# Performance work log

Hardware: AMD Instinct MI355X
Metric: run time of the kernel (lower is better)

Reference implementation:

```python
import jax, jax.numpy as jnp
import numpy as np

N = 50000; E = 800000; H = 4; C = 64; FEAT = 128; EDIM = 16; G = 256
NEG_SLOPE = 0.2; BN_EPS = 1e-5


def _gat_layer(x, src, dst, W, a_src, a_dst, bias, gamma, beta, alpha_edge=None):
    # GATConv (concat=True, PyG math), then BatchNorm1d (batch stats) + ReLU.
    h = (x @ W).reshape(N, H, C)                       # [N,H,C]
    alpha = (h * a_src).sum(-1)[src] + (h * a_dst).sum(-1)[dst]   # [Etot,H]
    if alpha_edge is not None:
        alpha = alpha + alpha_edge
    alpha = jax.nn.leaky_relu(alpha, NEG_SLOPE)
    amax = jax.ops.segment_max(alpha, dst, num_segments=N)        # edge softmax over dst
    ea = jnp.exp(alpha - amax[dst])
    denom = jax.ops.segment_sum(ea, dst, num_segments=N)
    coef = ea / (denom[dst] + 1e-16)
    out = jax.ops.segment_sum(coef[:, :, None] * h[src], dst, num_segments=N)
    out = out.reshape(N, H * C) + bias
    mu = out.mean(0)
    var = out.var(0)
    out = (out - mu) / jnp.sqrt(var + BN_EPS) * gamma + beta
    return jax.nn.relu(out)


def setup_inputs() -> dict:
    key = jax.random.key(0)
    ks = jax.random.split(key, 32)
    s = 0.05
    inp = {
        "x": jax.random.normal(ks[0], (N, FEAT), jnp.float32),
        "edge_index": jax.random.randint(ks[1], (2, E), 0, N),
        "edge_attr": jax.random.normal(ks[2], (E, EDIM), jnp.float32),
        "batch": jnp.sort(jax.random.randint(ks[3], (N,), 0, G)),
    }
    in_dims = [FEAT, H * C, H * C]
    for i in range(3):
        k = 4 + 7 * i
        inp[f"W{i}"] = jax.random.normal(ks[k], (in_dims[i], H * C), jnp.float32) * s
        inp[f"att_src{i}"] = jax.random.normal(ks[k + 1], (H, C), jnp.float32) * s
        inp[f"att_dst{i}"] = jax.random.normal(ks[k + 2], (H, C), jnp.float32) * s
        inp[f"bias{i}"] = jnp.zeros((H * C,), jnp.float32)
        inp[f"gamma{i}"] = jnp.ones((H * C,), jnp.float32)
        inp[f"beta{i}"] = jnp.zeros((H * C,), jnp.float32)
    inp["We0"] = jax.random.normal(ks[28], (EDIM, H * C), jnp.float32) * s
    inp["att_e0"] = jax.random.normal(ks[29], (H, C), jnp.float32) * s
    return inp


def reference(x, edge_index, edge_attr, batch,
              W0, att_src0, att_dst0, bias0, gamma0, beta0,
              W1, att_src1, att_dst1, bias1, gamma1, beta1,
              W2, att_src2, att_dst2, bias2, gamma2, beta2,
              We0, att_e0):
    # PyG GATConv adds self-loops; edge_attr for self-loops filled with mean.
    loops = jnp.arange(N)
    src = jnp.concatenate([edge_index[0], loops])
    dst = jnp.concatenate([edge_index[1], loops])
    ea_sl = jnp.concatenate([edge_attr, jnp.broadcast_to(edge_attr.mean(0), (N, EDIM))], 0)
    e = (ea_sl @ We0).reshape(E + N, H, C)
    alpha_e = (e * att_e0).sum(-1)                     # [Etot,H]
    x = _gat_layer(x, src, dst, W0, att_src0, att_dst0, bias0, gamma0, beta0, alpha_e)
    x = _gat_layer(x, src, dst, W1, att_src1, att_dst1, bias1, gamma1, beta1)
    x = _gat_layer(x, src, dst, W2, att_src2, att_dst2, bias2, gamma2, beta2)
    # global_mean_pool
    counts = jax.ops.segment_sum(jnp.ones((N,), x.dtype), batch, num_segments=G)
    sums = jax.ops.segment_sum(x, batch, num_segments=G)
    return sums / jnp.clip(counts, 1.0)[:, None]
```

## Files before the change

### kernel.cpp

```cpp
#include <hip/hip_runtime.h>
#include <math.h>

#define NN 50000
#define NE 800000
#define ET 850000
#define HCC 256
#define GG 256
#define CAP 64
#define NB 16

constexpr int RTILES = 782;
constexpr int G0B    = 512;
constexpr int CSRB   = 416;

constexpr size_t NHC    = (size_t)NN * HCC;
constexpr size_t O_H    = 0;
constexpr size_t O_AGG  = O_H + NHC / 2;
constexpr size_t O_REC  = O_AGG + NHC / 2;
constexpr size_t O_BT0  = O_REC + (size_t)NN * CAP * 4;
constexpr size_t O_BT1  = O_BT0 + 16384;
constexpr size_t O_BT2  = O_BT1 + 32768;
constexpr size_t O_AS   = O_BT2 + 32768;
constexpr size_t O_AD   = O_AS + (size_t)NN * 4;
constexpr size_t O_M    = O_AD + (size_t)NN * 4;
constexpr size_t O_ZERO = O_M + 64;
constexpr size_t O_DEG  = O_ZERO;
constexpr size_t O_SLS  = O_DEG + NN;
constexpr size_t O_PART = O_SLS + 4;
constexpr size_t O_END  = O_PART + 3 * NB * 512;
constexpr size_t ZWORDS = O_END - O_ZERO;
constexpr int    ZBLK   = (int)((ZWORDS / 4 + 255) / 256);

typedef __attribute__((ext_vector_type(8))) short bf16x8;
typedef __attribute__((ext_vector_type(4))) float f32x4;

__device__ inline unsigned short f2bf(float f) {
    unsigned int u = __float_as_uint(f);
    unsigned int r = (u + 0x7fffu + ((u >> 16) & 1u)) >> 16;
    return (unsigned short)r;
}
__device__ inline float b2f(unsigned short u) {
    return __uint_as_float(((unsigned int)u) << 16);
}
__device__ inline float bflo(unsigned int u) { return __uint_as_float(u << 16); }
__device__ inline float bfhi(unsigned int u) { return __uint_as_float(u & 0xffff0000u); }

__global__ void prep_kernel(const float* __restrict__ W0, const float* __restrict__ W1,
                            const float* __restrict__ W2,
                            const float* __restrict__ We0, const float* __restrict__ att_e0,
                            unsigned short* __restrict__ Bt0,
                            unsigned short* __restrict__ Bt1,
                            unsigned short* __restrict__ Bt2,
                            float* __restrict__ M, float* __restrict__ zbase) {
    int b = blockIdx.x;
    if (b >= 641) {
        size_t idx = ((size_t)(b - 641) * 256 + threadIdx.x) * 4;
        if (idx < ZWORDS)
            *(float4*)(zbase + idx) = make_float4(0.f, 0.f, 0.f, 0.f);
        return;
    }
    if (b == 640) {
        int t = threadIdx.x;
        if (t < 64) {
            int k = t >> 2, hh = t & 3;
            float s = 0.f;
            for (int c = 0; c < 64; ++c)
                s += We0[k * 256 + hh * 64 + c] * att_e0[hh * 64 + c];
            M[k * 4 + hh] = s;
        }
        return;
    }
    const float* W; unsigned short* Bt; int K, base;
    if (b < 128)      { W = W0; Bt = Bt0; K = 128; base = 0; }
    else if (b < 384) { W = W1; Bt = Bt1; K = 256; base = 128; }
    else              { W = W2; Bt = Bt2; K = 256; base = 384; }
    int idx = (b - base) * 256 + threadIdx.x;
    int n = idx & 255, k = idx >> 8;
    Bt[(size_t)n * K + k] = f2bf(W[(size_t)k * 256 + n]);
}

__global__ __launch_bounds__(512) void g0csr(const float* __restrict__ xf,
                                             const unsigned short* __restrict__ Bt,
                                             const float* __restrict__ att_src,
                                             const float* __restrict__ att_dst,
                                             unsigned short* __restrict__ Hout,
                                             float* __restrict__ asA,
                                             float* __restrict__ adA,
                                             const int* __restrict__ srcA,
                                             const int* __restrict__ dstA,
                                             const float* __restrict__ ea,
                                             const float* __restrict__ Mm,
                                             int* __restrict__ deg,
                                             uint4* __restrict__ rec,
                                             float* __restrict__ slsum) {
    constexpr int K  = 128;
    constexpr int KP = K + 8;
    __shared__ unsigned short Bs[128][KP];
    __shared__ unsigned short As[2][64][KP];
    __shared__ float prt[8][4];

    int tid = threadIdx.x;
    int wave = tid >> 6, lane = tid & 63;

    if (blockIdx.x >= G0B) {
        int t0 = (int)(blockIdx.x - G0B) * 2048 + tid;
        float a0 = 0.f, a1 = 0.f, a2 = 0.f, a3 = 0.f;
        #pragma unroll
        for (int q = 0; q < 4; ++q) {
            int e = t0 + q * 512;
            if (e < ET) {
                bool real = (e < NE);
                int d = real ? dstA[e] : (e - NE);
                int s = real ? srcA[e] : (e - NE);
                int p = atomicAdd(&deg[d], 1);
                if (p > CAP - 1) p = CAP - 1;
                int slot = d * CAP + p;
                uint4 r;
                r.z = (unsigned)s;
                if (real) {
                    r.w = 0u;
                    const float4* pp = (const float4*)(ea + (size_t)e * 16);
                    float4 va = pp[0], vb = pp[1], vc = pp[2], vd = pp[3];
                    float v[16] = {va.x, va.y, va.z, va.w, vb.x, vb.y, vb.z, vb.w,
                                   vc.x, vc.y, vc.z, vc.w, vd.x, vd.y, vd.z, vd.w};
                    float o0 = 0.f, o1 = 0.f, o2 = 0.f, o3 = 0.f;
                    #pragma unroll
                    for (int k = 0; k < 16; ++k) {
                        float4 m4 = *(const float4*)(Mm + k * 4);
                        o0 = fmaf(v[k], m4.x, o0);
                        o1 = fmaf(v[k], m4.y, o1);
                        o2 = fmaf(v[k], m4.z, o2);
                        o3 = fmaf(v[k], m4.w, o3);
                    }
                    r.x = ((unsigned)f2bf(o1) << 16) | (unsigned)f2bf(o0);
                    r.y = ((unsigned)f2bf(o3) << 16) | (unsigned)f2bf(o2);
                    a0 += o0; a1 += o1; a2 += o2; a3 += o3;
                } else {
                    r.x = 0u; r.y = 0u; r.w = 1u;
                }
                rec[slot] = r;
            }
        }
        #pragma unroll
        for (int off = 32; off; off >>= 1) {
            a0 += __shfl_xor(a0, off);
            a1 += __shfl_xor(a1, off);
            a2 += __shfl_xor(a2, off);
            a3 += __shfl_xor(a3, off);
        }
        if (lane == 0) {
            prt[wave][0] = a0; prt[wave][1] = a1;
            prt[wave][2] = a2; prt[wave][3] = a3;
        }
        __syncthreads();
        if (tid < 4) {
            float s = 0.f;
            #pragma unroll
            for (int w = 0; w < 8; ++w) s += prt[w][tid];
            atomicAdd(&slsum[tid], s);
        }
        return;
    }

    int quad = lane >> 4, l16 = lane & 15;
    int wr = wave >> 1, wc = wave & 1;

    int b = blockIdx.x;
    int cb = (b >> 3) & 1;
    int ts = ((b >> 4) << 3) | (b & 7);
    const int np = G0B >> 1;
    int colbase = cb * 128;
    int head = cb * 2 + wc;

    {
        constexpr int TOT = 128 * K;
        for (int idx = tid * 8; idx < TOT; idx += 4096) {
            int br = idx / K, bk = idx % K;
            uint4 v = *(const uint4*)(Bt + (size_t)(colbase + br) * K + bk);
            *(uint4*)&Bs[br][bk] = v;
        }
    }

    int srow = tid >> 3;
    const int scol0 = (tid & 7) * 16;

    float4 ldA_[4], ldB_[4];

    auto issue = [&](float4 (&ld)[4], int t) {
        int r = t * 64 + srow;
        if (r < NN) {
            const float4* src = (const float4*)(xf + (size_t)r * K + scol0);
            #pragma unroll
            for (int q = 0; q < 4; ++q) ld[q] = src[q];
        } else {
            #pragma unroll
            for (int q = 0; q < 4; ++q) ld[q] = make_float4(0.f, 0.f, 0.f, 0.f);
        }
    };
    auto commit = [&](float4 (&ld)[4], int buf) {
        #pragma unroll
        for (int q = 0; q < 2; ++q) {
            float4 a = ld[2 * q], c = ld[2 * q + 1];
            uint4 v;
            v.x = ((unsigned)f2bf(a.y) << 16) | f2bf(a.x);
            v.y = ((unsigned)f2bf(a.w) << 16) | f2bf(a.z);
            v.z = ((unsigned)f2bf(c.y) << 16) | f2bf(c.x);
            v.w = ((unsigned)f2bf(c.w) << 16) | f2bf(c.z);
            *(uint4*)&As[buf][srow][scol0 + q * 8] = v;
        }
    };

    float asc[4], adc_[4];
    #pragma unroll
    for (int ni = 0; ni < 4; ++ni) {
        int c = colbase + wc * 64 + ni * 16 + l16;
        asc[ni]  = att_src[c];
        adc_[ni] = att_dst[c];
    }

    int t = ts;
    issue(ldA_, t);
    asm volatile("s_waitcnt lgkmcnt(0)" ::: "memory");
    __builtin_amdgcn_s_barrier();

    auto tilestep = [&](float4 (&ldCur)[4], float4 (&ldNxt)[4], int buf, int t_, int tn) {
        if (tn < RTILES) issue(ldNxt, tn);
        commit(ldCur, buf);
        asm volatile("s_waitcnt lgkmcnt(0)" ::: "memory");
        __builtin_amdgcn_s_barrier();

        f32x4 acc[4] = {};
        #pragma unroll
        for (int k0 = 0; k0 < K; k0 += 32) {
            bf16x8 af, bfr[4];
            af = *(const bf16x8*)&As[buf][wr * 16 + l16][k0 + quad * 8];
            #pragma unroll
            for (int ni = 0; ni < 4; ++ni)
                bfr[ni] = *(const bf16x8*)&Bs[wc * 64 + ni * 16 + l16][k0 + quad * 8];
            #pragma unroll
            for (int ni = 0; ni < 4; ++ni)
                acc[ni] = __builtin_amdgcn_mfma_f32_16x16x32_bf16(
                    af, bfr[ni], acc[ni], 0, 0, 0);
        }
        int row0 = t_ * 64 + wr * 16;
        #pragma unroll
        for (int reg = 0; reg < 4; ++reg) {
            int r = row0 + quad * 4 + reg;
            if (r < NN) {
                #pragma unroll
                for (int ni = 0; ni < 4; ++ni) {
                    int c = colbase + wc * 64 + ni * 16 + l16;
                    Hout[(size_t)r * HCC + c] = f2bf(acc[ni][reg]);
                }
            }
            float s1 = acc[0][reg] * asc[0] + acc[1][reg] * asc[1] +
                       acc[2][reg] * asc[2] + acc[3][reg] * asc[3];
            float d1 = acc[0][reg] * adc_[0] + acc[1][reg] * adc_[1] +
                       acc[2][reg] * adc_[2] + acc[3][reg] * adc_[3];
            #pragma unroll
            for (int off = 1; off < 16; off <<= 1) {
                s1 += __shfl_xor(s1, off);
                d1 += __shfl_xor(d1, off);
            }
            if (l16 == 0 && r < NN) {
                asA[(size_t)r * 4 + head] = s1;
                adA[(size_t)r * 4 + head] = d1;
            }
        }
    };

    while (t < RTILES) {
        int t1 = t + np;
        tilestep(ldA_, ldB_, 0, t, t1);
        t = t1;
        if (t >= RTILES) break;
        int t2 = t + np;
        tilestep(ldB_, ldA_, 1, t, t2);
        t = t2;
    }
}

template <int K, bool NORM>
__global__ __launch_bounds__(512) void gemm2(const unsigned short* __restrict__ Ab,
                                             const unsigned short* __restrict__ Bt,
                                             const float* __restrict__ part,
                                             const float* __restrict__ gamma,
                                             const float* __restrict__ beta,
                                             const float* __restrict__ att_src,
                                             const float* __restrict__ att_dst,
                                             unsigned short* __restrict__ Hout,
                                             float* __restrict__ asA,
                                             float* __restrict__ adA, int M) {
    constexpr int KP  = K + 8;
    constexpr int NLD = K / 64;
    __shared__ unsigned short Bs[128][KP];
    __shared__ unsigned short As[2][64][KP];
    __shared__ float kvs[256], cvs[256];

    int tid = threadIdx.x;
    int wave = tid >> 6, lane = tid & 63;
    int quad = lane >> 4, l16 = lane & 15;
    int wr = wave >> 1, wc = wave & 1;

    int b = blockIdx.x;
    int cb = (b >> 3) & 1;
    int ts = ((b >> 4) << 3) | (b & 7);
    int np = (int)(gridDim.x >> 1);
    int colbase = cb * 128;
    int head = cb * 2 + wc;

    if (NORM) {
        if (tid < 256) {
            int ch = tid;
            float s = 0.f, s2 = 0.f;
            #pragma unroll
            for (int q = 0; q < NB; ++q) {
                s  += part[q * 512 + ch];
                s2 += part[q * 512 + 256 + ch];
            }
            const float invN = 1.0f / (float)NN;
            float mr = s * invN;
            float var = s2 * invN - mr * mr;
            float k = gamma[ch] * rsqrtf(var + 1e-5f);
            kvs[ch] = k;
            cvs[ch] = beta[ch] - mr * k;
        }
    }
    {
        constexpr int TOT = 128 * K;
        for (int idx = tid * 8; idx < TOT; idx += 4096) {
            int br = idx / K, bk = idx % K;
            uint4 v = *(const uint4*)(Bt + (size_t)(colbase + br) * K + bk);
            *(uint4*)&Bs[br][bk] = v;
        }
    }

    int srow = tid >> 3;
    const int scol0 = (tid & 7) * (K / 8);

    uint4 ldA_[NLD], ldB_[NLD];

    auto issue = [&](uint4 (&ld)[NLD], int t) {
        int r = t * 64 + srow;
        if (r < M) {
            const uint4* src = (const uint4*)(Ab + (size_t)r * K + scol0);
            #pragma unroll
            for (int q = 0; q < NLD; ++q) ld[q] = src[q];
        } else {
            #pragma unroll
            for (int q = 0; q < NLD; ++q) ld[q] = make_uint4(0u, 0u, 0u, 0u);
        }
    };
    auto commit = [&](uint4 (&ld)[NLD], int buf) {
        #pragma unroll
        for (int q = 0; q < NLD; ++q) {
            uint4 v = ld[q];
            if (NORM) {
                int ch = scol0 + q * 8;
                float u[8] = {bflo(v.x), bfhi(v.x), bflo(v.y), bfhi(v.y),
                              bflo(v.z), bfhi(v.z), bflo(v.w), bfhi(v.w)};
                #pragma unroll
                for (int j = 0; j < 8; ++j)
                    u[j] = fmaxf(fmaf(u[j], kvs[ch + j], cvs[ch + j]), 0.f);
                v.x = ((unsigned)f2bf(u[1]) << 16) | f2bf(u[0]);
                v.y = ((unsigned)f2bf(u[3]) << 16) | f2bf(u[2]);
                v.z = ((unsigned)f2bf(u[5]) << 16) | f2bf(u[4]);
                v.w = ((unsigned)f2bf(u[7]) << 16) | f2bf(u[6]);
            }
            *(uint4*)&As[buf][srow][scol0 + q * 8] = v;
        }
    };

    float asc[4], adc_[4];
    #pragma unroll
    for (int ni = 0; ni < 4; ++ni) {
        int c = colbase + wc * 64 + ni * 16 + l16;
        asc[ni]  = att_src[c];
        adc_[ni] = att_dst[c];
    }

    int t = ts;
    issue(ldA_, t);
    asm volatile("s_waitcnt lgkmcnt(0)" ::: "memory");
    __builtin_amdgcn_s_barrier();

    auto tilestep = [&](uint4 (&ldCur)[NLD], uint4 (&ldNxt)[NLD], int buf, int t_, int tn) {
        if (tn < RTILES) issue(ldNxt, tn);
        commit(ldCur, buf);
        asm volatile("s_waitcnt lgkmcnt(0)" ::: "memory");
        __builtin_amdgcn_s_barrier();

        f32x4 acc[4] = {};
        #pragma unroll
        for (int k0 = 0; k0 < K; k0 += 32) {
            bf16x8 af, bfr[4];
            af = *(const bf16x8*)&As[buf][wr * 16 + l16][k0 + quad * 8];
            #pragma unroll
            for (int ni = 0; ni < 4; ++ni)
                bfr[ni] = *(const bf16x8*)&Bs[wc * 64 + ni * 16 + l16][k0 + quad * 8];
            #pragma unroll
            for (int ni = 0; ni < 4; ++ni)
                acc[ni] = __builtin_amdgcn_mfma_f32_16x16x32_bf16(
                    af, bfr[ni], acc[ni], 0, 0, 0);
        }
        int row0 = t_ * 64 + wr * 16;
        #pragma unroll
        for (int reg = 0; reg < 4; ++reg) {
            int r = row0 + quad * 4 + reg;
            if (r < M) {
                #pragma unroll
                for (int ni = 0; ni < 4; ++ni) {
                    int c = colbase + wc * 64 + ni * 16 + l16;
                    Hout[(size_t)r * HCC + c] = f2bf(acc[ni][reg]);
                }
            }
            float s1 = acc[0][reg] * asc[0] + acc[1][reg] * asc[1] +
                       acc[2][reg] * asc[2] + acc[3][reg] * asc[3];
            float d1 = acc[0][reg] * adc_[0] + acc[1][reg] * adc_[1] +
                       acc[2][reg] * adc_[2] + acc[3][reg] * adc_[3];
            #pragma unroll
            for (int off = 1; off < 16; off <<= 1) {
                s1 += __shfl_xor(s1, off);
                d1 += __shfl_xor(d1, off);
            }
            if (l16 == 0 && r < M) {
                asA[(size_t)r * 4 + head] = s1;
                adA[(size_t)r * 4 + head] = d1;
            }
        }
    };

    while (t < RTILES) {
        int t1 = t + np;
        tilestep(ldA_, ldB_, 0, t, t1);
        t = t1;
        if (t >= RTILES) break;
        int t2 = t + np;
        tilestep(ldB_, ldA_, 1, t, t2);
        t = t2;
    }
}

template <bool HAS_AE>
__global__ __launch_bounds__(512) void agg_kernel(const unsigned short* __restrict__ Hm,
                                                  const float* __restrict__ asA,
                                                  const float* __restrict__ adA,
                                                  const uint4* __restrict__ rec,
                                                  const int* __restrict__ degA,
                                                  const float* __restrict__ slsum,
                                                  unsigned short* __restrict__ outA,
                                                  float* __restrict__ part) {
    __shared__ float wlds[8][260];
    __shared__ float slds[2][8][256];
    int wave = threadIdx.x >> 6, lane = threadIdx.x & 63;
    int n = blockIdx.x * 8 + wave;
    int head = lane >> 4;
    int st = n * CAP;
    int d = degA[n];
    if (d > CAP) d = CAP;
    float4 ad4 = *(const float4*)(adA + (size_t)n * 4);

    float4 w4 = make_float4(0.f, 0.f, 0.f, 0.f);
    int ms = 0;
    if (lane < d) {
        uint4 r = rec[st + lane];
        ms = (int)r.z;
        float4 av = *(const float4*)(asA + (size_t)ms * 4);
        float4 t = make_float4(av.x + ad4.x, av.y + ad4.y, av.z + ad4.z, av.w + ad4.w);
        if (HAS_AE) {
            if (r.w) {
                const float inv = 1.0f / (float)NE;
                t.x += slsum[0] * inv; t.y += slsum[1] * inv;
                t.z += slsum[2] * inv; t.w += slsum[3] * inv;
            } else {
                t.x += bflo(r.x); t.y += bfhi(r.x);
                t.z += bflo(r.y); t.w += bfhi(r.y);
            }
        }
        t.x = (t.x > 0.f) ? t.x : 0.2f * t.x;
        t.y = (t.y > 0.f) ? t.y : 0.2f * t.y;
        t.z = (t.z > 0.f) ? t.z : 0.2f * t.z;
        t.w = (t.w > 0.f) ? t.w : 0.2f * t.w;
        w4.x = __expf(t.x);
        w4.y = __expf(t.y);
        w4.z = __expf(t.z);
        w4.w = __expf(t.w);
    }
    float4 Dv = w4;
    wlds[wave][0 * 65 + lane] = w4.x;
    wlds[wave][1 * 65 + lane] = w4.y;
    wlds[wave][2 * 65 + lane] = w4.z;
    wlds[wave][3 * 65 + lane] = w4.w;

    float4 acc = make_float4(0.f, 0.f, 0.f, 0.f);
    const unsigned short* hb = Hm + lane * 4;
    int cnt8 = (d + 7) & ~7;
    const float* wrow = &wlds[wave][head * 65];

    int sjA[8]; ushort4 hvA[8];
    #pragma unroll
    for (int q = 0; q < 8; ++q)
        sjA[q] = __builtin_amdgcn_readlane(ms, q);
    #pragma unroll
    for (int q = 0; q < 8; ++q)
        hvA[q] = *(const ushort4*)(hb + (size_t)sjA[q] * HCC);
    for (int jj = 0; jj < cnt8; jj += 8) {
        int nj = jj + 8;
        bool more = (nj < cnt8);
        ushort4 hvB[8];
        if (more) {
            int sjB[8];
            #pragma unroll
            for (int q = 0; q < 8; ++q)
                sjB[q] = __builtin_amdgcn_readlane(ms, nj + q);
            #pragma unroll
            for (int q = 0; q < 8; ++q)
                hvB[q] = *(const ushort4*)(hb + (size_t)sjB[q] * HCC);
        }
        float wq[8];
        #pragma unroll
        for (int q = 0; q < 8; ++q)
            wq[q] = wrow[jj + q];
        #pragma unroll
        for (int q = 0; q < 8; ++q) {
            acc.x = fmaf(wq[q], b2f(hvA[q].x), acc.x);
            acc.y = fmaf(wq[q], b2f(hvA[q].y), acc.y);
            acc.z = fmaf(wq[q], b2f(hvA[q].z), acc.z);
            acc.w = fmaf(wq[q], b2f(hvA[q].w), acc.w);
        }
        if (more) {
            #pragma unroll
            for (int q = 0; q < 8; ++q)
                hvA[q] = hvB[q];
        }
    }
    #pragma unroll
    for (int off = 32; off; off >>= 1) {
        Dv.x += __shfl_xor(Dv.x, off);
        Dv.y += __shfl_xor(Dv.y, off);
        Dv.z += __shfl_xor(Dv.z, off);
        Dv.w += __shfl_xor(Dv.w, off);
    }
    float D = (head & 2) ? ((head & 1) ? Dv.w : Dv.z) : ((head & 1) ? Dv.y : Dv.x);
    float inv = 1.0f / (D + 1e-16f);
    float4 o = make_float4(acc.x * inv, acc.y * inv, acc.z * inv, acc.w * inv);
    ushort4 ob = make_ushort4(f2bf(o.x), f2bf(o.y), f2bf(o.z), f2bf(o.w));
    *(ushort4*)(outA + (size_t)n * HCC + lane * 4) = ob;

    *(float4*)&slds[0][wave][lane * 4] = o;
    *(float4*)&slds[1][wave][lane * 4] =
        make_float4(o.x * o.x, o.y * o.y, o.z * o.z, o.w * o.w);
    __syncthreads();
    int t = threadIdx.x;
    if (t < 512) {
        int ch = t & 255, which = t >> 8;
        float s = 0.f;
        #pragma unroll
        for (int w = 0; w < 8; ++w)
            s += slds[which][w][ch];
        int bucket = blockIdx.x & (NB - 1);
        atomicAdd(&part[bucket * 512 + which * 256 + ch], s);
    }
}

__global__ void pool_kernel(const unsigned short* __restrict__ aggb,
                            const float* __restrict__ part,
                            const float* __restrict__ gamma, const float* __restrict__ beta,
                            const int* __restrict__ batch,
                            float* __restrict__ out) {
    int ch = threadIdx.x;
    int g = blockIdx.x;
    float s = 0.f, s2 = 0.f;
    #pragma unroll
    for (int b = 0; b < NB; ++b) {
        s  += part[b * 512 + ch];
        s2 += part[b * 512 + 256 + ch];
    }
    const float invN = 1.0f / (float)NN;
    float mr = s * invN;
    float var = s2 * invN - mr * mr;
    float k = gamma[ch] * rsqrtf(var + 1e-5f);
    float c = beta[ch] - mr * k;

    int lo = 0, hi = NN;
    while (lo < hi) { int mid = (lo + hi) >> 1; if (batch[mid] < g) lo = mid + 1; else hi = mid; }
    int start = lo;
    lo = start; hi = NN;
    while (lo < hi) { int mid = (lo + hi) >> 1; if (batch[mid] < g + 1) lo = mid + 1; else hi = mid; }
    int end = lo;

    float a0 = 0.f, a1 = 0.f, a2 = 0.f, a3 = 0.f;
    int n = start;
    for (; n + 3 < end; n += 4) {
        a0 += fmaxf(fmaf(b2f(aggb[(size_t)n * HCC + ch]), k, c), 0.f);
        a1 += fmaxf(fmaf(b2f(aggb[(size_t)(n + 1) * HCC + ch]), k, c), 0.f);
        a2 += fmaxf(fmaf(b2f(aggb[(size_t)(n + 2) * HCC + ch]), k, c), 0.f);
        a3 += fmaxf(fmaf(b2f(aggb[(size_t)(n + 3) * HCC + ch]), k, c), 0.f);
    }
    for (; n < end; ++n)
        a0 += fmaxf(fmaf(b2f(aggb[(size_t)n * HCC + ch]), k, c), 0.f);
    float tot = (a0 + a1) + (a2 + a3);
    out[(size_t)g * HCC + ch] = tot / fmaxf((float)(end - start), 1.0f);
}

extern "C" void kernel_launch(void* const* d_in, const int* in_sizes, int n_in,
                              void* d_out, int out_size, void* d_ws, size_t ws_size,
                              hipStream_t stream) {
    const float* x = (const float*)d_in[0];
    const int* edge_index = (const int*)d_in[1];
    const int* srcA = edge_index;
    const int* dstA = edge_index + NE;
    const float* edge_attr = (const float*)d_in[2];
    const int* batch = (const int*)d_in[3];
    const float* W[3]   = {(const float*)d_in[4],  (const float*)d_in[10], (const float*)d_in[16]};
    const float* asc[3] = {(const float*)d_in[5],  (const float*)d_in[11], (const float*)d_in[17]};
    const float* adc[3] = {(const float*)d_in[6],  (const float*)d_in[12], (const float*)d_in[18]};
    const float* gam[3] = {(const float*)d_in[8],  (const float*)d_in[14], (const float*)d_in[20]};
    const float* bet[3] = {(const float*)d_in[9],  (const float*)d_in[15], (const float*)d_in[21]};
    const float* We0 = (const float*)d_in[22];
    const float* att_e0 = (const float*)d_in[23];

    float* wsf = (float*)d_ws;
    unsigned short* hbuf = (unsigned short*)(wsf + O_H);
    unsigned short* aggb = (unsigned short*)(wsf + O_AGG);
    uint4* rec   = (uint4*)(wsf + O_REC);
    unsigned short* Bt0  = (unsigned short*)(wsf + O_BT0);
    unsigned short* Bt1  = (unsigned short*)(wsf + O_BT1);
    unsigned short* Bt2  = (unsigned short*)(wsf + O_BT2);
    float* asA   = wsf + O_AS;
    float* adA   = wsf + O_AD;
    float* Mb    = wsf + O_M;
    int*   deg   = (int*)(wsf + O_DEG);
    float* slsum = wsf + O_SLS;
    float* part  = wsf + O_PART;

    prep_kernel<<<641 + ZBLK, 256, 0, stream>>>(W[0], W[1], W[2], We0, att_e0,
                                                Bt0, Bt1, Bt2, Mb, wsf + O_ZERO);

    g0csr<<<G0B + CSRB, 512, 0, stream>>>(x, Bt0, asc[0], adc[0], hbuf, asA, adA,
                                          srcA, dstA, edge_attr, Mb, deg, rec, slsum);
    agg_kernel<true><<<6250, 512, 0, stream>>>(hbuf, asA, adA, rec, deg, slsum,
        aggb, part + (size_t)0 * NB * 512);

    gemm2<256, true><<<256, 512, 0, stream>>>(aggb, Bt1, part + (size_t)0 * NB * 512,
        gam[0], bet[0], asc[1], adc[1], hbuf, asA, adA, NN);
    agg_kernel<false><<<6250, 512, 0, stream>>>(hbuf, asA, adA, rec, deg, slsum,
        aggb, part + (size_t)1 * NB * 512);

    gemm2<256, true><<<256, 512, 0, stream>>>(aggb, Bt2, part + (size_t)1 * NB * 512,
        gam[1], bet[1], asc[2], adc[2], hbuf, asA, adA, NN);
    agg_kernel<false><<<6250, 512, 0, stream>>>(hbuf, asA, adA, rec, deg, slsum,
        aggb, part + (size_t)2 * NB * 512);

    pool_kernel<<<GG, 256, 0, stream>>>(aggb, part + (size_t)2 * NB * 512,
                                        gam[2], bet[2], batch, (float*)d_out);
}
```

Baseline: 494.6 us.

## Split layer-1/2 GEMM into 64-column head tiles and interleave CSR blocks in g0csr

The layer 1 and 2 GEMM moves from 128-column tiles on 256 blocks to 64-column (one head) tiles on 512 blocks. This halves the LDS footprint (B tile and a single A buffer) so more blocks fit per CU. The attention dot products are now combined across the two waves through shared memory and an extra barrier. Separately, the CSR-building blocks in g0csr are interleaved with the GEMM blocks by block index parity so the two kinds of work run concurrently instead of CSR blocks being scheduled last. The costs are that the A matrix is re-read by four column groups instead of two, the BN-normalize work is duplicated, and each tile needs an extra barrier.

```diff
diff --git a/kernel.cpp b/kernel.cpp
--- a/kernel.cpp
+++ b/kernel.cpp
@@ -102,8 +102,11 @@
     int tid = threadIdx.x;
     int wave = tid >> 6, lane = tid & 63;
 
-    if (blockIdx.x >= G0B) {
-        int t0 = (int)(blockIdx.x - G0B) * 2048 + tid;
+    int braw = blockIdx.x;
+    bool is_csr = (braw & 1) && (braw < 2 * CSRB);
+
+    if (is_csr) {
+        int t0 = (braw >> 1) * 2048 + tid;
         float a0 = 0.f, a1 = 0.f, a2 = 0.f, a3 = 0.f;
         #pragma unroll
         for (int q = 0; q < 4; ++q) {
@@ -162,10 +165,10 @@
         return;
     }
 
+    int b = (braw < 2 * CSRB) ? (braw >> 1) : (braw - CSRB);
     int quad = lane >> 4, l16 = lane & 15;
     int wr = wave >> 1, wc = wave & 1;
 
-    int b = blockIdx.x;
     int cb = (b >> 3) & 1;
     int ts = ((b >> 4) << 3) | (b & 7);
     const int np = G0B >> 1;
@@ -280,22 +283,23 @@
     }
 }
 
-template <int K, bool NORM>
-__global__ __launch_bounds__(512) void gemm2(const unsigned short* __restrict__ Ab,
-                                             const unsigned short* __restrict__ Bt,
-                                             const float* __restrict__ part,
-                                             const float* __restrict__ gamma,
-                                             const float* __restrict__ beta,
-                                             const float* __restrict__ att_src,
-                                             const float* __restrict__ att_dst,
-                                             unsigned short* __restrict__ Hout,
-                                             float* __restrict__ asA,
-                                             float* __restrict__ adA, int M) {
+template <int K>
+__global__ __launch_bounds__(512) void gemm2b(const unsigned short* __restrict__ Ab,
+                                              const unsigned short* __restrict__ Bt,
+                                              const float* __restrict__ part,
+                                              const float* __restrict__ gamma,
+                                              const float* __restrict__ beta,
+                                              const float* __restrict__ att_src,
+                                              const float* __restrict__ att_dst,
+                                              unsigned short* __restrict__ Hout,
+                                              float* __restrict__ asA,
+                                              float* __restrict__ adA) {
     constexpr int KP  = K + 8;
     constexpr int NLD = K / 64;
-    __shared__ unsigned short Bs[128][KP];
-    __shared__ unsigned short As[2][64][KP];
+    __shared__ unsigned short Bs[64][KP];
+    __shared__ unsigned short As[64][KP];
     __shared__ float kvs[256], cvs[256];
+    __shared__ float sps[2][2][64];
 
     int tid = threadIdx.x;
     int wave = tid >> 6, lane = tid & 63;
@@ -303,13 +307,13 @@
     int wr = wave >> 1, wc = wave & 1;
 
     int b = blockIdx.x;
-    int cb = (b >> 3) & 1;
-    int ts = ((b >> 4) << 3) | (b & 7);
-    int np = (int)(gridDim.x >> 1);
-    int colbase = cb * 128;
-    int head = cb * 2 + wc;
-
-    if (NORM) {
+    int quarter = (b >> 3) & 3;
+    int rowgrp  = ((b >> 5) << 3) | (b & 7);
+    int colbase = quarter * 64;
+    int head = quarter;
+    const int np = 128;
+
+    {
         if (tid < 256) {
             int ch = tid;
             float s = 0.f, s2 = 0.f;
@@ -327,7 +331,7 @@
         }
     }
     {
-        constexpr int TOT = 128 * K;
+        constexpr int TOT = 64 * K;
         for (int idx = tid * 8; idx < TOT; idx += 4096) {
             int br = idx / K, bk = idx % K;
             uint4 v = *(const uint4*)(Bt + (size_t)(colbase + br) * K + bk);
@@ -342,7 +346,7 @@
 
     auto issue = [&](uint4 (&ld)[NLD], int t) {
         int r = t * 64 + srow;
-        if (r < M) {
+        if (r < NN) {
             const uint4* src = (const uint4*)(Ab + (size_t)r * K + scol0);
             #pragma unroll
             for (int q = 0; q < NLD; ++q) ld[q] = src[q];
@@ -351,92 +355,94 @@
             for (int q = 0; q < NLD; ++q) ld[q] = make_uint4(0u, 0u, 0u, 0u);
         }
     };
-    auto commit = [&](uint4 (&ld)[NLD], int buf) {
+    auto commit = [&](uint4 (&ld)[NLD]) {
         #pragma unroll
         for (int q = 0; q < NLD; ++q) {
             uint4 v = ld[q];
-            if (NORM) {
-                int ch = scol0 + q * 8;
-                float u[8] = {bflo(v.x), bfhi(v.x), bflo(v.y), bfhi(v.y),
-                              bflo(v.z), bfhi(v.z), bflo(v.w), bfhi(v.w)};
-                #pragma unroll
-                for (int j = 0; j < 8; ++j)
-                    u[j] = fmaxf(fmaf(u[j], kvs[ch + j], cvs[ch + j]), 0.f);
-                v.x = ((unsigned)f2bf(u[1]) << 16) | f2bf(u[0]);
-                v.y = ((unsigned)f2bf(u[3]) << 16) | f2bf(u[2]);
-                v.z = ((unsigned)f2bf(u[5]) << 16) | f2bf(u[4]);
-                v.w = ((unsigned)f2bf(u[7]) << 16) | f2bf(u[6]);
-            }
-            *(uint4*)&As[buf][srow][scol0 + q * 8] = v;
+            int ch = scol0 + q * 8;
+            float u[8] = {bflo(v.x), bfhi(v.x), bflo(v.y), bfhi(v.y),
+                          bflo(v.z), bfhi(v.z), bflo(v.w), bfhi(v.w)};
+            #pragma unroll
+            for (int j = 0; j < 8; ++j)
+                u[j] = fmaxf(fmaf(u[j], kvs[ch + j], cvs[ch + j]), 0.f);
+            v.x = ((unsigned)f2bf(u[1]) << 16) | f2bf(u[0]);
+            v.y = ((unsigned)f2bf(u[3]) << 16) | f2bf(u[2]);
+            v.z = ((unsigned)f2bf(u[5]) << 16) | f2bf(u[4]);
+            v.w = ((unsigned)f2bf(u[7]) << 16) | f2bf(u[6]);
+            *(uint4*)&As[srow][scol0 + q * 8] = v;
         }
     };
 
-    float asc[4], adc_[4];
+    float asc[2], adc_[2];
     #pragma unroll
-    for (int ni = 0; ni < 4; ++ni) {
-        int c = colbase + wc * 64 + ni * 16 + l16;
+    for (int ni = 0; ni < 2; ++ni) {
+        int c = colbase + wc * 32 + ni * 16 + l16;
         asc[ni]  = att_src[c];
         adc_[ni] = att_dst[c];
     }
 
-    int t = ts;
+    int t = rowgrp;
     issue(ldA_, t);
     asm volatile("s_waitcnt lgkmcnt(0)" ::: "memory");
     __builtin_amdgcn_s_barrier();
 
-    auto tilestep = [&](uint4 (&ldCur)[NLD], uint4 (&ldNxt)[NLD], int buf, int t_, int tn) {
+    auto tilestep = [&](uint4 (&ldCur)[NLD], uint4 (&ldNxt)[NLD], int t_, int tn) {
         if (tn < RTILES) issue(ldNxt, tn);
-        commit(ldCur, buf);
+        commit(ldCur);
         asm volatile("s_waitcnt lgkmcnt(0)" ::: "memory");
         __builtin_amdgcn_s_barrier();
 
-        f32x4 acc[4] = {};
+        f32x4 acc[2] = {};
         #pragma unroll
         for (int k0 = 0; k0 < K; k0 += 32) {
-            bf16x8 af, bfr[4];
-            af = *(const bf16x8*)&As[buf][wr * 16 + l16][k0 + quad * 8];
-            #pragma unroll
-            for (int ni = 0; ni < 4; ++ni)
-                bfr[ni] = *(const bf16x8*)&Bs[wc * 64 + ni * 16 + l16][k0 + quad * 8];
-            #pragma unroll
-            for (int ni = 0; ni < 4; ++ni)
-                acc[ni] = __builtin_amdgcn_mfma_f32_16x16x32_bf16(
-                    af, bfr[ni], acc[ni], 0, 0, 0);
-        }
+            bf16x8 af = *(const bf16x8*)&As[wr * 16 + l16][k0 + quad * 8];
+            bf16x8 b0 = *(const bf16x8*)&Bs[wc * 32 + l16][k0 + quad * 8];
+            bf16x8 b1 = *(const bf16x8*)&Bs[wc * 32 + 16 + l16][k0 + quad * 8];
+            acc[0] = __builtin_amdgcn_mfma_f32_16x16x32_bf16(af, b0, acc[0], 0, 0, 0);
+            acc[1] = __builtin_amdgcn_mfma_f32_16x16x32_bf16(af, b1, acc[1], 0, 0, 0);
+        }
+
         int row0 = t_ * 64 + wr * 16;
         #pragma unroll
         for (int reg = 0; reg < 4; ++reg) {
             int r = row0 + quad * 4 + reg;
-            if (r < M) {
-                #pragma unroll
-                for (int ni = 0; ni < 4; ++ni) {
-                    int c = colbase + wc * 64 + ni * 16 + l16;
-                    Hout[(size_t)r * HCC + c] = f2bf(acc[ni][reg]);
-                }
-            }
-            float s1 = acc[0][reg] * asc[0] + acc[1][reg] * asc[1] +
-                       acc[2][reg] * asc[2] + acc[3][reg] * asc[3];
-            float d1 = acc[0][reg] * adc_[0] + acc[1][reg] * adc_[1] +
-                       acc[2][reg] * adc_[2] + acc[3][reg] * adc_[3];
+            if (r < NN) {
+                Hout[(size_t)r * HCC + colbase + wc * 32 + l16]      = f2bf(acc[0][reg]);
+                Hout[(size_t)r * HCC + colbase + wc * 32 + 16 + l16] = f2bf(acc[1][reg]);
+            }
+            float s1 = acc[0][reg] * asc[0] + acc[1][reg] * asc[1];
+            float d1 = acc[0][reg] * adc_[0] + acc[1][reg] * adc_[1];
             #pragma unroll
             for (int off = 1; off < 16; off <<= 1) {
                 s1 += __shfl_xor(s1, off);
                 d1 += __shfl_xor(d1, off);
             }
-            if (l16 == 0 && r < M) {
-                asA[(size_t)r * 4 + head] = s1;
-                adA[(size_t)r * 4 + head] = d1;
+            if (l16 == 0) {
+                sps[wc][0][wr * 16 + quad * 4 + reg] = s1;
+                sps[wc][1][wr * 16 + quad * 4 + reg] = d1;
+            }
+        }
+
+        asm volatile("s_waitcnt lgkmcnt(0)" ::: "memory");
+        __builtin_amdgcn_s_barrier();
+
+        if (tid < 128) {
+            int row = tid & 63, sd = tid >> 6;
+            int r = t_ * 64 + row;
+            if (r < NN) {
+                float v = sps[0][sd][row] + sps[1][sd][row];
+                (sd ? adA : asA)[(size_t)r * 4 + head] = v;
             }
         }
     };
 
     while (t < RTILES) {
         int t1 = t + np;
-        tilestep(ldA_, ldB_, 0, t, t1);
+        tilestep(ldA_, ldB_, t, t1);
         t = t1;
         if (t >= RTILES) break;
         int t2 = t + np;
-        tilestep(ldB_, ldA_, 1, t, t2);
+        tilestep(ldB_, ldA_, t, t2);
         t = t2;
     }
 }
@@ -642,13 +648,13 @@
     agg_kernel<true><<<6250, 512, 0, stream>>>(hbuf, asA, adA, rec, deg, slsum,
         aggb, part + (size_t)0 * NB * 512);
 
-    gemm2<256, true><<<256, 512, 0, stream>>>(aggb, Bt1, part + (size_t)0 * NB * 512,
-        gam[0], bet[0], asc[1], adc[1], hbuf, asA, adA, NN);
+    gemm2b<256><<<512, 512, 0, stream>>>(aggb, Bt1, part + (size_t)0 * NB * 512,
+        gam[0], bet[0], asc[1], adc[1], hbuf, asA, adA);
     agg_kernel<false><<<6250, 512, 0, stream>>>(hbuf, asA, adA, rec, deg, slsum,
         aggb, part + (size_t)1 * NB * 512);
 
-    gemm2<256, true><<<256, 512, 0, stream>>>(aggb, Bt2, part + (size_t)1 * NB * 512,
-        gam[1], bet[1], asc[2], adc[2], hbuf, asA, adA, NN);
+    gemm2b<256><<<512, 512, 0, stream>>>(aggb, Bt2, part + (size_t)1 * NB * 512,
+        gam[1], bet[1], asc[2], adc[2], hbuf, asA, adA);
     agg_kernel<false><<<6250, 512, 0, stream>>>(hbuf, asA, adA, rec, deg, slsum,
         aggb, part + (size_t)2 * NB * 512);
 
```

Result: slower. 533.3 us (+7.8%).
